# Performance work log

Hardware: AMD Instinct MI355X
Metric: run time of the kernel (lower is better)

The kernel has to match this reference:

```python
import jax, jax.numpy as jnp
import numpy as np

ALPHA = 0.1
BETA = 1.1
NUM_CLASSES = 16
EPS = 1e-8  # matches torch cosine_similarity eps
BATCH = 131072
DIM = 512


def setup_inputs() -> dict:
    key = jax.random.key(0)
    k1, k2 = jax.random.split(key)
    embeddings = jax.random.normal(k1, (BATCH, DIM), dtype=jnp.float32)
    labels = jax.random.randint(k2, (BATCH,), 0, NUM_CLASSES)
    return {"embeddings": embeddings, "labels": labels}


def _cos_dist(a, b):
    # a: [M, D], b: [N, D] -> 1 - cosine_similarity, shape [M, N]
    an = a / jnp.maximum(jnp.linalg.norm(a, axis=-1, keepdims=True), EPS)
    bn = b / jnp.maximum(jnp.linalg.norm(b, axis=-1, keepdims=True), EPS)
    return 1.0 - an @ bn.T


def reference(embeddings, labels):
    C = NUM_CLASSES
    N = embeddings.shape[0]
    dt = embeddings.dtype

    # class centroids (dummy anchors) via scatter-mean
    cnt = jax.ops.segment_sum(jnp.ones((N,), dt), labels, num_segments=C)  # [C]
    sums = jax.ops.segment_sum(embeddings, labels, num_segments=C)        # [C, D]
    centroids = sums / jnp.maximum(cnt, 1.0)[:, None]
    present = cnt > 0

    # close class pairs: i < j, both present, centroid distance <= beta
    pd = _cos_dist(centroids, centroids)                    # [C, C]
    upper = jnp.triu(jnp.ones((C, C), bool), k=1)
    pairmask = upper & (pd <= BETA) & present[:, None] & present[None, :]
    pm = pairmask.astype(dt)
    deg = pm.sum(1) + pm.sum(0)                             # pairs involving each class

    # distances from every centroid to every sample
    D = _cos_dist(centroids, embeddings)                    # [C, N]

    # intra: each sample of class c contributes relu(d(cent_c, x) - alpha),
    # once per close pair involving c
    d_own = D[labels, jnp.arange(N)]                        # [N]
    intra_sum = jnp.sum(deg[labels] * jax.nn.relu(d_own - ALPHA))

    # inter: S[c, c'] = sum over samples with label c' of relu(beta - d(cent_c, x))
    S = jax.ops.segment_sum(jax.nn.relu(BETA - D).T, labels, num_segments=C).T  # [C, C]
    inter_sum = jnp.sum(pm * (S + S.T))

    # number of terms in each loss list: sum over pairs of (cnt_i + cnt_j)
    count = jnp.sum(deg * cnt)
    denom = jnp.maximum(count, 1.0)
    num_pairs = pm.sum()

    loss = jnp.where(num_pairs > 0, intra_sum / denom + inter_sum / denom, 0.0)
    return loss
```

## Files before the change

kernel.cpp:

```cpp
#include <hip/hip_runtime.h>

constexpr float kAlpha = 0.1f;
constexpr float kBeta  = 1.1f;
constexpr int   kC     = 16;
constexpr int   kD     = 512;
constexpr float kEps   = 1e-8f;

constexpr int SUMS_OFF = 0;
constexpr int CNT_OFF  = 8192;
constexpr int TOT_OFF  = 8208;
constexpr int CN_OFF   = 8224;
constexpr int MSK_OFF  = 16416;
constexpr int SCL_OFF  = 16432;
constexpr int ZERO_FLOATS = 8209;

__device__ __forceinline__ float dot4(float4 a, float4 b) {
    return a.x * b.x + a.y * b.y + a.z * b.z + a.w * b.w;
}

__global__ __launch_bounds__(512) void k1_sums(const float* __restrict__ emb,
                                               const int* __restrict__ labels,
                                               float* __restrict__ sums,
                                               float* __restrict__ cnt,
                                               int N, int rpb) {
    __shared__ float lacc[kC * kD];
    __shared__ float lcnt[kC];
    int tid = threadIdx.x;
    int wave = tid >> 6, lane = tid & 63;
    int half = wave & 1;

    for (int i = tid; i < kC * kD; i += 512) lacc[i] = 0.f;
    if (tid < kC) lcnt[tid] = 0.f;
    __syncthreads();

    float4 acc[kC];
#pragma unroll
    for (int c = 0; c < kC; ++c) acc[c] = make_float4(0.f, 0.f, 0.f, 0.f);
    float cacc = 0.f;

    const float4* e4 = (const float4*)emb;
    long long h0 = 2LL * blockIdx.x * rpb;
    long long hEnd = min(h0 + 2LL * rpb, 2LL * (long long)N);

    for (long long h = h0 + wave; h < hEnd; h += 16) {
        long long hb = h + 8;
        bool vb = (hb < hEnd);
        int rowA = (int)(h >> 1);
        int rowB = vb ? (int)(hb >> 1) : rowA;
        int lA = labels[rowA];
        int lB = labels[rowB];
        float4 vA = e4[(size_t)rowA * 128 + half * 64 + lane];
        float4 vB = e4[(size_t)rowB * 128 + half * 64 + lane];
        if (!vb) vB = make_float4(0.f, 0.f, 0.f, 0.f);
#pragma unroll
        for (int c = 0; c < kC; ++c) {
            if (lA == c) { acc[c].x += vA.x; acc[c].y += vA.y; acc[c].z += vA.z; acc[c].w += vA.w; }
            if (lB == c) { acc[c].x += vB.x; acc[c].y += vB.y; acc[c].z += vB.z; acc[c].w += vB.w; }
        }
        if (half == 0 && lane < kC) {
            cacc += (lA == lane ? 1.f : 0.f) + ((vb && lB == lane) ? 1.f : 0.f);
        }
    }

#pragma unroll
    for (int c = 0; c < kC; ++c) {
        float* p = &lacc[c * kD + half * 256 + lane * 4];
        atomicAdd(p + 0, acc[c].x);
        atomicAdd(p + 1, acc[c].y);
        atomicAdd(p + 2, acc[c].z);
        atomicAdd(p + 3, acc[c].w);
    }
    if (half == 0 && lane < kC) atomicAdd(&lcnt[lane], cacc);
    __syncthreads();
    for (int i = tid; i < kC * kD; i += 512) atomicAdd(&sums[i], lacc[i]);
    if (tid < kC) atomicAdd(&cnt[tid], lcnt[tid]);
}

__global__ __launch_bounds__(256) void k2_cent(const float* __restrict__ sums,
                                               const float* __restrict__ cnt_g,
                                               float* __restrict__ cn_g,
                                               unsigned* __restrict__ mask_g,
                                               float* __restrict__ scal) {
    __shared__ __align__(16) float lcn[kC * kD];
    __shared__ float lcnt[kC];
    __shared__ float red[256];
    __shared__ float norms[kC];
    __shared__ float pdm[kC * kC];
    int tid = threadIdx.x;
    if (tid < kC) lcnt[tid] = cnt_g[tid];
    __syncthreads();

    int c = tid >> 4, sub = tid & 15;
    float invc = 1.f / fmaxf(lcnt[c], 1.f);
    float sq = 0.f;
    for (int d = sub; d < kD; d += 16) {
        float v = sums[c * kD + d] * invc;
        lcn[c * kD + d] = v;
        sq += v * v;
    }
    red[tid] = sq;
    __syncthreads();
    if (tid < kC) {
        float t = 0.f;
        for (int k = 0; k < 16; ++k) t += red[tid * 16 + k];
        norms[tid] = fmaxf(sqrtf(t), kEps);
    }
    __syncthreads();
    for (int i = tid; i < kC * kD; i += 256) {
        float v = lcn[i] / norms[i / kD];
        lcn[i] = v;
        cn_g[i] = v;
    }
    __syncthreads();
    int pi = tid >> 4, pj = tid & 15;
    float dot = 0.f;
    for (int dd = 0; dd < kD; ++dd) {
        int d = (dd + tid) & (kD - 1);
        dot += lcn[pi * kD + d] * lcn[pj * kD + d];
    }
    pdm[tid] = 1.f - dot;
    __syncthreads();
    if (tid == 0) {
        unsigned m[kC];
        for (int a = 0; a < kC; ++a) m[a] = 0u;
        float npairs = 0.f;
        for (int a = 0; a < kC; ++a)
            for (int b = a + 1; b < kC; ++b) {
                bool close = (pdm[a * kC + b] <= kBeta) && (lcnt[a] > 0.f) && (lcnt[b] > 0.f);
                if (close) { m[a] |= 1u << b; m[b] |= 1u << a; npairs += 1.f; }
            }
        float count = 0.f;
        for (int a = 0; a < kC; ++a) {
            mask_g[a] = m[a];
            count += (float)__popc(m[a]) * lcnt[a];
        }
        scal[0] = fmaxf(count, 1.f);
        scal[1] = npairs;
    }
}

constexpr int TR = 32;
__global__ __launch_bounds__(512, 2) void k3_main(const float* __restrict__ emb,
                                                  const int* __restrict__ labels,
                                                  const float* __restrict__ cn_g,
                                                  const unsigned* __restrict__ mask_g,
                                                  float* __restrict__ total,
                                                  int N, int rpb) {
    __shared__ __align__(16) float4 xbuf[TR * 128];
    __shared__ unsigned lmask[kC];
    __shared__ float wsum[8];
    int tid = threadIdx.x;
    int wave = tid >> 6, lane = tid & 63;
    int g = lane >> 4, j = lane & 15;

    const float4* w4 = (const float4*)cn_g;
    float4 wreg[4][8];
#pragma unroll
    for (int c = 0; c < 4; ++c)
#pragma unroll
        for (int i = 0; i < 8; ++i)
            wreg[c][i] = w4[(4 * g + c) * 128 + i * 16 + j];
    if (tid < kC) lmask[tid] = mask_g[tid];

    int r0 = blockIdx.x * rpb;
    int r1 = min(r0 + rpb, N);
    float priv = 0.f;

    const float4* src = (const float4*)emb;
    float4 st[8];

    if (r0 < r1) {
        int avail = (r1 - r0) * 128;
#pragma unroll
        for (int k = 0; k < 8; ++k) {
            int idx = k * 512 + tid;
            st[k] = (idx < avail) ? src[(size_t)r0 * 128 + idx] : make_float4(0.f, 0.f, 0.f, 0.f);
        }
#pragma unroll
        for (int k = 0; k < 8; ++k) xbuf[k * 512 + tid] = st[k];
    }
    __syncthreads();

    for (int rt = r0; rt < r1; rt += TR) {
        int ntile = rt + TR;
        bool more = (ntile < r1);
        if (more) {
            int avail = (r1 - ntile) * 128;
#pragma unroll
            for (int k = 0; k < 8; ++k) {
                int idx = k * 512 + tid;
                st[k] = (idx < avail) ? src[(size_t)ntile * 128 + idx] : make_float4(0.f, 0.f, 0.f, 0.f);
            }
        }

        int rows = min(TR, r1 - rt);
        for (int rr = wave; rr < rows; rr += 8) {
            int row = rt + rr;
            int lab = labels[row];
            const float4* xr = &xbuf[rr * 128];
            float d0 = 0.f, d1 = 0.f, d2 = 0.f, d3 = 0.f, nrm = 0.f;
#pragma unroll
            for (int i = 0; i < 8; ++i) {
                float4 x = xr[i * 16 + j];
                nrm += dot4(x, x);
                d0 += dot4(x, wreg[0][i]);
                d1 += dot4(x, wreg[1][i]);
                d2 += dot4(x, wreg[2][i]);
                d3 += dot4(x, wreg[3][i]);
            }
#pragma unroll
            for (int m = 1; m < 16; m <<= 1) {
                d0 += __shfl_xor(d0, m, 64);
                d1 += __shfl_xor(d1, m, 64);
                d2 += __shfl_xor(d2, m, 64);
                d3 += __shfl_xor(d3, m, 64);
                nrm += __shfl_xor(nrm, m, 64);
            }
            if (j == 0) {
                unsigned mm = lmask[lab];
                float inv = 1.f / fmaxf(sqrtf(nrm), kEps);
                float s = 0.f;
                float dv[4] = {d0, d1, d2, d3};
#pragma unroll
                for (int c = 0; c < 4; ++c) {
                    int cg = 4 * g + c;
                    float dd = 1.f - dv[c] * inv;
                    if ((mm >> cg) & 1u) s += fmaxf(kBeta - dd, 0.f);
                    if (cg == lab) s += (float)__popc(mm) * fmaxf(dd - kAlpha, 0.f);
                }
                priv += s;
            }
        }
        __syncthreads();
        if (more) {
#pragma unroll
            for (int k = 0; k < 8; ++k) xbuf[k * 512 + tid] = st[k];
        }
        __syncthreads();
    }

#pragma unroll
    for (int off = 32; off > 0; off >>= 1) priv += __shfl_down(priv, off, 64);
    if (lane == 0) wsum[wave] = priv;
    __syncthreads();
    if (tid == 0) {
        float t = 0.f;
#pragma unroll
        for (int w = 0; w < 8; ++w) t += wsum[w];
        atomicAdd(total, t);
    }
}

__global__ void k4_final(const float* __restrict__ total,
                         const float* __restrict__ scal,
                         float* __restrict__ out) {
    out[0] = (scal[1] > 0.f) ? (total[0] / scal[0]) : 0.f;
}

extern "C" void kernel_launch(void* const* d_in, const int* in_sizes, int n_in,
                              void* d_out, int out_size, void* d_ws, size_t ws_size,
                              hipStream_t stream) {
    const float* emb = (const float*)d_in[0];
    const int* labels = (const int*)d_in[1];
    int N = in_sizes[0] / kD;

    float* ws = (float*)d_ws;
    float* sums = ws + SUMS_OFF;
    float* cnt = ws + CNT_OFF;
    float* total = ws + TOT_OFF;
    float* cn = ws + CN_OFF;
    unsigned* mask = (unsigned*)(ws + MSK_OFF);
    float* scal = ws + SCL_OFF;

    hipMemsetAsync(d_ws, 0, ZERO_FLOATS * sizeof(float), stream);

    int blocks1 = 512;
    int rpb1 = (N + blocks1 - 1) / blocks1;
    k1_sums<<<blocks1, 512, 0, stream>>>(emb, labels, sums, cnt, N, rpb1);

    k2_cent<<<1, 256, 0, stream>>>(sums, cnt, cn, mask, scal);

    int blocks3 = 256;
    int rpb3 = (N + blocks3 - 1) / blocks3;
    k3_main<<<blocks3, 512, 0, stream>>>(emb, labels, cn, mask, total, N, rpb3);

    k4_final<<<1, 1, 0, stream>>>(total, scal, (float*)d_out);
}
```

Before: 559.2 us.

## Use LDS atomics in class-sum kernel and register double-buffering in main kernel

The class-sum kernel stops keeping 16 per-class float4 register accumulators with a branchy select. Each wave now loads a whole row and does wave-uniform LDS atomic adds into that row's class slot, using a permuted layout that is un-permuted on the global flush. The block count is doubled. The main kernel drops its shared-memory tile staging and __syncthreads, and each wave loads rows straight into registers with ping-pong prefetch of the next row. The aim is lower register pressure, fewer barriers and better overlap of loads with compute, at the cost of heavy LDS atomic traffic and smaller per-wave prefetch depth.

New measurement: 699.3 us. 25.1% more time.

```diff
diff --git a/kernel.cpp b/kernel.cpp
--- a/kernel.cpp
+++ b/kernel.cpp
@@ -27,52 +27,61 @@
     __shared__ float lcnt[kC];
     int tid = threadIdx.x;
     int wave = tid >> 6, lane = tid & 63;
-    int half = wave & 1;
 
     for (int i = tid; i < kC * kD; i += 512) lacc[i] = 0.f;
     if (tid < kC) lcnt[tid] = 0.f;
     __syncthreads();
 
-    float4 acc[kC];
-#pragma unroll
-    for (int c = 0; c < kC; ++c) acc[c] = make_float4(0.f, 0.f, 0.f, 0.f);
-    float cacc = 0.f;
-
     const float4* e4 = (const float4*)emb;
-    long long h0 = 2LL * blockIdx.x * rpb;
-    long long hEnd = min(h0 + 2LL * rpb, 2LL * (long long)N);
-
-    for (long long h = h0 + wave; h < hEnd; h += 16) {
-        long long hb = h + 8;
-        bool vb = (hb < hEnd);
-        int rowA = (int)(h >> 1);
-        int rowB = vb ? (int)(hb >> 1) : rowA;
-        int lA = labels[rowA];
-        int lB = labels[rowB];
-        float4 vA = e4[(size_t)rowA * 128 + half * 64 + lane];
-        float4 vB = e4[(size_t)rowB * 128 + half * 64 + lane];
-        if (!vb) vB = make_float4(0.f, 0.f, 0.f, 0.f);
-#pragma unroll
-        for (int c = 0; c < kC; ++c) {
-            if (lA == c) { acc[c].x += vA.x; acc[c].y += vA.y; acc[c].z += vA.z; acc[c].w += vA.w; }
-            if (lB == c) { acc[c].x += vB.x; acc[c].y += vB.y; acc[c].z += vB.z; acc[c].w += vB.w; }
+    int r0 = blockIdx.x * rpb;
+    int r1 = min(r0 + rpb, N);
+
+    for (int r = r0 + wave; r < r1; r += 16) {
+        int rb = r + 8;
+        bool vb = rb < r1;
+        int rbi = vb ? rb : r;
+
+        float4 a0 = e4[(size_t)r * 128 + lane];
+        float4 a1 = e4[(size_t)r * 128 + 64 + lane];
+        float4 b0 = e4[(size_t)rbi * 128 + lane];
+        float4 b1 = e4[(size_t)rbi * 128 + 64 + lane];
+        int la = __builtin_amdgcn_readfirstlane(labels[r]);
+        int lb = __builtin_amdgcn_readfirstlane(labels[rbi]);
+
+        float* pa = &lacc[la * kD];
+        atomicAdd(&pa[      lane], a0.x);
+        atomicAdd(&pa[ 64 + lane], a0.y);
+        atomicAdd(&pa[128 + lane], a0.z);
+        atomicAdd(&pa[192 + lane], a0.w);
+        atomicAdd(&pa[256 + lane], a1.x);
+        atomicAdd(&pa[320 + lane], a1.y);
+        atomicAdd(&pa[384 + lane], a1.z);
+        atomicAdd(&pa[448 + lane], a1.w);
+        if (lane == 0) atomicAdd(&lcnt[la], 1.f);
+
+        if (vb) {
+            float* pb = &lacc[lb * kD];
+            atomicAdd(&pb[      lane], b0.x);
+            atomicAdd(&pb[ 64 + lane], b0.y);
+            atomicAdd(&pb[128 + lane], b0.z);
+            atomicAdd(&pb[192 + lane], b0.w);
+            atomicAdd(&pb[256 + lane], b1.x);
+            atomicAdd(&pb[320 + lane], b1.y);
+            atomicAdd(&pb[384 + lane], b1.z);
+            atomicAdd(&pb[448 + lane], b1.w);
+            if (lane == 0) atomicAdd(&lcnt[lb], 1.f);
         }
-        if (half == 0 && lane < kC) {
-            cacc += (lA == lane ? 1.f : 0.f) + ((vb && lB == lane) ? 1.f : 0.f);
-        }
-    }
-
-#pragma unroll
-    for (int c = 0; c < kC; ++c) {
-        float* p = &lacc[c * kD + half * 256 + lane * 4];
-        atomicAdd(p + 0, acc[c].x);
-        atomicAdd(p + 1, acc[c].y);
-        atomicAdd(p + 2, acc[c].z);
-        atomicAdd(p + 3, acc[c].w);
-    }
-    if (half == 0 && lane < kC) atomicAdd(&lcnt[lane], cacc);
-    __syncthreads();
-    for (int i = tid; i < kC * kD; i += 512) atomicAdd(&sums[i], lacc[i]);
+    }
+    __syncthreads();
+
+    for (int gidx = tid; gidx < kC * kD; gidx += 512) {
+        int c = gidx >> 9;
+        int d = gidx & 511;
+        int half = d >> 8;
+        int u = d & 255;
+        int l = u >> 2, k = u & 3;
+        atomicAdd(&sums[gidx], lacc[c * 512 + half * 256 + k * 64 + l]);
+    }
     if (tid < kC) atomicAdd(&cnt[tid], lcnt[tid]);
 }
 
@@ -139,14 +148,12 @@
     }
 }
 
-constexpr int TR = 32;
 __global__ __launch_bounds__(512, 2) void k3_main(const float* __restrict__ emb,
                                                   const int* __restrict__ labels,
                                                   const float* __restrict__ cn_g,
                                                   const unsigned* __restrict__ mask_g,
                                                   float* __restrict__ total,
                                                   int N, int rpb) {
-    __shared__ __align__(16) float4 xbuf[TR * 128];
     __shared__ unsigned lmask[kC];
     __shared__ float wsum[8];
     int tid = threadIdx.x;
@@ -161,83 +168,79 @@
         for (int i = 0; i < 8; ++i)
             wreg[c][i] = w4[(4 * g + c) * 128 + i * 16 + j];
     if (tid < kC) lmask[tid] = mask_g[tid];
+    __syncthreads();
 
     int r0 = blockIdx.x * rpb;
     int r1 = min(r0 + rpb, N);
+    const float4* src = (const float4*)emb;
     float priv = 0.f;
 
-    const float4* src = (const float4*)emb;
-    float4 st[8];
-
-    if (r0 < r1) {
-        int avail = (r1 - r0) * 128;
-#pragma unroll
-        for (int k = 0; k < 8; ++k) {
-            int idx = k * 512 + tid;
-            st[k] = (idx < avail) ? src[(size_t)r0 * 128 + idx] : make_float4(0.f, 0.f, 0.f, 0.f);
+#define K3_COMPUTE(X, LAB)                                                     \
+    do {                                                                       \
+        float d0 = 0.f, d1 = 0.f, d2 = 0.f, d3 = 0.f, nrm = 0.f;               \
+        _Pragma("unroll")                                                      \
+        for (int i = 0; i < 8; ++i) {                                          \
+            float4 x = X[i];                                                   \
+            nrm += dot4(x, x);                                                 \
+            d0 += dot4(x, wreg[0][i]);                                         \
+            d1 += dot4(x, wreg[1][i]);                                         \
+            d2 += dot4(x, wreg[2][i]);                                         \
+            d3 += dot4(x, wreg[3][i]);                                         \
+        }                                                                      \
+        _Pragma("unroll")                                                      \
+        for (int m = 1; m < 16; m <<= 1) {                                     \
+            d0 += __shfl_xor(d0, m, 64);                                       \
+            d1 += __shfl_xor(d1, m, 64);                                       \
+            d2 += __shfl_xor(d2, m, 64);                                       \
+            d3 += __shfl_xor(d3, m, 64);                                       \
+            nrm += __shfl_xor(nrm, m, 64);                                     \
+        }                                                                      \
+        if (j == 0) {                                                          \
+            unsigned mm = lmask[LAB];                                          \
+            float inv = 1.f / fmaxf(sqrtf(nrm), kEps);                         \
+            float dv[4] = {d0, d1, d2, d3};                                    \
+            float s = 0.f;                                                     \
+            _Pragma("unroll")                                                  \
+            for (int c = 0; c < 4; ++c) {                                      \
+                int cg = 4 * g + c;                                            \
+                float dd = 1.f - dv[c] * inv;                                  \
+                if ((mm >> cg) & 1u) s += fmaxf(kBeta - dd, 0.f);              \
+                if (cg == LAB) s += (float)__popc(mm) * fmaxf(dd - kAlpha, 0.f);\
+            }                                                                  \
+            priv += s;                                                         \
+        }                                                                      \
+    } while (0)
+
+    int rA = r0 + wave;
+    if (rA < r1) {
+        float4 xA[8], xB[8];
+        int laA, laB;
+#pragma unroll
+        for (int i = 0; i < 8; ++i) xA[i] = src[(size_t)rA * 128 + i * 16 + j];
+        laA = labels[rA];
+        int rB = rA + 8;
+        while (true) {
+            bool vB = rB < r1;
+            int rBi = vB ? rB : rA;
+#pragma unroll
+            for (int i = 0; i < 8; ++i) xB[i] = src[(size_t)rBi * 128 + i * 16 + j];
+            laB = labels[rBi];
+            K3_COMPUTE(xA, laA);
+            if (!vB) break;
+
+            int rN = rB + 8;
+            bool vN = rN < r1;
+            int rNi = vN ? rN : rB;
+#pragma unroll
+            for (int i = 0; i < 8; ++i) xA[i] = src[(size_t)rNi * 128 + i * 16 + j];
+            laA = labels[rNi];
+            K3_COMPUTE(xB, laB);
+            if (!vN) break;
+            rA = rN;
+            rB = rN + 8;
         }
-#pragma unroll
-        for (int k = 0; k < 8; ++k) xbuf[k * 512 + tid] = st[k];
-    }
-    __syncthreads();
-
-    for (int rt = r0; rt < r1; rt += TR) {
-        int ntile = rt + TR;
-        bool more = (ntile < r1);
-        if (more) {
-            int avail = (r1 - ntile) * 128;
-#pragma unroll
-            for (int k = 0; k < 8; ++k) {
-                int idx = k * 512 + tid;
-                st[k] = (idx < avail) ? src[(size_t)ntile * 128 + idx] : make_float4(0.f, 0.f, 0.f, 0.f);
-            }
-        }
-
-        int rows = min(TR, r1 - rt);
-        for (int rr = wave; rr < rows; rr += 8) {
-            int row = rt + rr;
-            int lab = labels[row];
-            const float4* xr = &xbuf[rr * 128];
-            float d0 = 0.f, d1 = 0.f, d2 = 0.f, d3 = 0.f, nrm = 0.f;
-#pragma unroll
-            for (int i = 0; i < 8; ++i) {
-                float4 x = xr[i * 16 + j];
-                nrm += dot4(x, x);
-                d0 += dot4(x, wreg[0][i]);
-                d1 += dot4(x, wreg[1][i]);
-                d2 += dot4(x, wreg[2][i]);
-                d3 += dot4(x, wreg[3][i]);
-            }
-#pragma unroll
-            for (int m = 1; m < 16; m <<= 1) {
-                d0 += __shfl_xor(d0, m, 64);
-                d1 += __shfl_xor(d1, m, 64);
-                d2 += __shfl_xor(d2, m, 64);
-                d3 += __shfl_xor(d3, m, 64);
-                nrm += __shfl_xor(nrm, m, 64);
-            }
-            if (j == 0) {
-                unsigned mm = lmask[lab];
-                float inv = 1.f / fmaxf(sqrtf(nrm), kEps);
-                float s = 0.f;
-                float dv[4] = {d0, d1, d2, d3};
-#pragma unroll
-                for (int c = 0; c < 4; ++c) {
-                    int cg = 4 * g + c;
-                    float dd = 1.f - dv[c] * inv;
-                    if ((mm >> cg) & 1u) s += fmaxf(kBeta - dd, 0.f);
-                    if (cg == lab) s += (float)__popc(mm) * fmaxf(dd - kAlpha, 0.f);
-                }
-                priv += s;
-            }
-        }
-        __syncthreads();
-        if (more) {
-#pragma unroll
-            for (int k = 0; k < 8; ++k) xbuf[k * 512 + tid] = st[k];
-        }
-        __syncthreads();
-    }
+    }
+#undef K3_COMPUTE
 
 #pragma unroll
     for (int off = 32; off > 0; off >>= 1) priv += __shfl_down(priv, off, 64);
@@ -274,7 +277,7 @@
 
     hipMemsetAsync(d_ws, 0, ZERO_FLOATS * sizeof(float), stream);
 
-    int blocks1 = 512;
+    int blocks1 = 1024;
     int rpb1 = (N + blocks1 - 1) / blocks1;
     k1_sums<<<blocks1, 512, 0, stream>>>(emb, labels, sums, cnt, N, rpb1);
 
```
